# Performance work log

Hardware: AMD Instinct MI355X
Metric: run time of the kernel (lower is better)

## Reference

```python
import jax, jax.numpy as jnp
import numpy as np

D_MODEL = 1024
N_HEADS = 16
HEAD_DIM = D_MODEL // N_HEADS
SEQ_LEN = 2048
BATCH = 2
THETA = 10000.0


def _rope_tables(dim, seq_len, theta=THETA):
    freqs = 1.0 / theta ** (jnp.arange(0, dim, 2, dtype=jnp.float32) / dim)  # (dim/2,)
    t = jnp.arange(seq_len, dtype=jnp.float32)
    ang = jnp.outer(t, freqs)  # (S, dim/2)
    # interleave each freq twice to match the (-x_odd, x_even) rotation layout
    cos = jnp.repeat(jnp.cos(ang), 2, axis=-1)  # (S, dim)
    sin = jnp.repeat(jnp.sin(ang), 2, axis=-1)
    return cos, sin


def _apply_rope(x, cos, sin):
    # x: (B, S, H, D); cos/sin: (S, D)
    x_rot = jnp.stack([-x[..., 1::2], x[..., ::2]], axis=-1).reshape(x.shape)
    return x * cos[None, :, None, :] + x_rot * sin[None, :, None, :]


def setup_inputs() -> dict:
    key = jax.random.key(0)
    ks = jax.random.split(key, 9)
    s = 1.0 / np.sqrt(D_MODEL)
    return {
        "x": jax.random.normal(ks[0], (BATCH, SEQ_LEN, D_MODEL), dtype=jnp.float32),
        "wq": jax.random.normal(ks[1], (D_MODEL, D_MODEL), jnp.float32) * s,
        "bq": jnp.zeros((D_MODEL,), jnp.float32),
        "wk": jax.random.normal(ks[2], (D_MODEL, D_MODEL), jnp.float32) * s,
        "bk": jnp.zeros((D_MODEL,), jnp.float32),
        "wv": jax.random.normal(ks[3], (D_MODEL, D_MODEL), jnp.float32) * s,
        "bv": jnp.zeros((D_MODEL,), jnp.float32),
        "wo": jax.random.normal(ks[4], (D_MODEL, D_MODEL), jnp.float32) * s,
        "bo": jnp.zeros((D_MODEL,), jnp.float32),
    }


def reference(x, wq, bq, wk, bk, wv, bv, wo, bo):
    B, S, _ = x.shape
    cos, sin = _rope_tables(HEAD_DIM, S)
    # projections (torch Linear: x @ W^T + b)
    q = (x @ wq.T + bq).reshape(B, S, N_HEADS, HEAD_DIM)
    k = (x @ wk.T + bk).reshape(B, S, N_HEADS, HEAD_DIM)
    v = (x @ wv.T + bv).reshape(B, S, N_HEADS, HEAD_DIM)
    q = _apply_rope(q, cos, sin)
    k = _apply_rope(k, cos, sin)
    # attention: bhqd, bhkd -> bhqk
    scale = 1.0 / np.sqrt(HEAD_DIM)
    scores = jnp.einsum("bqhd,bkhd->bhqk", q, k) * scale
    attn = jax.nn.softmax(scores, axis=-1)
    out = jnp.einsum("bhqk,bkhd->bqhd", attn, v).reshape(B, S, D_MODEL)
    return out @ wo.T + bo
```

## Files before the change

kernel.cpp:

```cpp
#include <hip/hip_runtime.h>

typedef __attribute__((ext_vector_type(8))) __bf16 bf16x8;
typedef __attribute__((ext_vector_type(4))) __bf16 bf16x4;
typedef __attribute__((ext_vector_type(4))) float f32x4;
typedef __attribute__((ext_vector_type(16))) float f32x16;
typedef __attribute__((ext_vector_type(4))) int i32x4;
typedef __attribute__((ext_vector_type(4))) unsigned short ushort4v;

__device__ __forceinline__ unsigned short f2bf(float f) {
  unsigned u = __builtin_bit_cast(unsigned, f);
  u += 0x7fffu + ((u >> 16) & 1u);
  return (unsigned short)(u >> 16);
}

__device__ __forceinline__ unsigned cvt_pk_bf16(float lo, float hi) {
  unsigned r;
  asm("v_cvt_pk_bf16_f32 %0, %1, %2" : "=v"(r) : "v"(lo), "v"(hi));
  return r;
}

__device__ __forceinline__ void pl32swap(unsigned& a, unsigned& b) {
  asm("v_permlane32_swap_b32 %0, %1" : "+v"(a), "+v"(b));
}

__device__ __forceinline__ void gload16(const void* g, void* l) {
  __builtin_amdgcn_global_load_lds(
      (const __attribute__((address_space(1))) void*)g,
      (__attribute__((address_space(3))) void*)l, 16, 0, 0);
}

__global__ __launch_bounds__(256) void convert_k(
    const float* __restrict__ x, const float* __restrict__ wq,
    const float* __restrict__ wk, const float* __restrict__ wv,
    const float* __restrict__ wo,
    unsigned short* __restrict__ xb, unsigned short* __restrict__ wqkv,
    unsigned short* __restrict__ wob, float* cosT, float* sinT) {
  if (blockIdx.x >= 8192) {
    const int idx = (blockIdx.x - 8192) * 256 + threadIdx.x;
    const int s = idx >> 5, j = idx & 31;
    const float freq = powf(10000.f, -(float)(2 * j) * (1.f / 64.f));
    const float ang = (float)s * freq;
    cosT[idx] = cosf(ang);
    sinT[idx] = sinf(ang);
    return;
  }
  const size_t i = ((size_t)blockIdx.x * 256 + threadIdx.x) * 4;
  const float* src; unsigned short* dst; size_t off;
  if (i < 4194304)      { src = x;  dst = xb;              off = i; }
  else if (i < 5242880) { src = wq; dst = wqkv;            off = i - 4194304; }
  else if (i < 6291456) { src = wk; dst = wqkv + 1048576;  off = i - 5242880; }
  else if (i < 7340032) { src = wv; dst = wqkv + 2097152;  off = i - 6291456; }
  else                  { src = wo; dst = wob;             off = i - 7340032; }
  f32x4 v = *(const f32x4*)(src + off);
  ushort4v o;
  o[0] = f2bf(v[0]); o[1] = f2bf(v[1]); o[2] = f2bf(v[2]); o[3] = f2bf(v[3]);
  *(ushort4v*)(dst + off) = o;
}

template <int EPI>
__global__ __launch_bounds__(256) void gemm_bt_k(
    const unsigned short* __restrict__ A, const unsigned short* __restrict__ B,
    int M, int N, int K,
    unsigned short* __restrict__ Qr, unsigned short* __restrict__ Kr,
    unsigned short* __restrict__ Vt,
    const float* __restrict__ bq, const float* __restrict__ bk,
    const float* __restrict__ bvv,
    const float* __restrict__ cosT, const float* __restrict__ sinT,
    float* __restrict__ Cout, const float* __restrict__ bias) {
  __shared__ char smem[65536];
  const int t = threadIdx.x;
  const int wave = t >> 6, lane = t & 63;
  const int l15 = lane & 15, g = lane >> 4;
  const int cpx = (int)gridDim.x >> 3;
  const int wg = (blockIdx.x & 7) * cpx + (blockIdx.x >> 3);
  const int nt = N >> 7;
  const int mb = (wg / nt) << 7;
  const int nb = (wg % nt) << 7;
  const int wm = (wave >> 1) << 6;
  const int wn = (wave & 1) << 6;

  const f32x4 zv = {0.f, 0.f, 0.f, 0.f};
  f32x4 acc[4][4];
#pragma unroll
  for (int i = 0; i < 4; i++)
#pragma unroll
    for (int j = 0; j < 4; j++) acc[i][j] = zv;

#pragma unroll
  for (int i = 0; i < 4; i++) {
    const int lin = t * 16 + i * 4096;
    const int r = lin >> 7;
    const int cb = (lin & 127) ^ ((r & 7) << 4);
    gload16((const char*)A + ((size_t)(mb + r) * K) * 2 + cb,
            smem + i * 4096 + wave * 1024);
    gload16((const char*)B + ((size_t)(nb + r) * K) * 2 + cb,
            smem + 16384 + i * 4096 + wave * 1024);
  }
  __syncthreads();

  int cur = 0;
  for (int kt = 0; kt < K; kt += 64) {
    const char* sc = smem + cur * 32768;
    if (kt + 64 < K) {
      char* sn = smem + (cur ^ 1) * 32768;
#pragma unroll
      for (int i = 0; i < 4; i++) {
        const int lin = t * 16 + i * 4096;
        const int r = lin >> 7;
        const int cb = (lin & 127) ^ ((r & 7) << 4);
        gload16((const char*)A + ((size_t)(mb + r) * K + kt + 64) * 2 + cb,
                sn + i * 4096 + wave * 1024);
        gload16((const char*)B + ((size_t)(nb + r) * K + kt + 64) * 2 + cb,
                sn + 16384 + i * 4096 + wave * 1024);
      }
    }

    bf16x8 af[4][2], bfr[4][2];
    const int sw = (l15 & 7) << 4;
#pragma unroll
    for (int mf = 0; mf < 4; mf++) {
      const int r = wm + mf * 16 + l15;
      const int r2 = wn + mf * 16 + l15;
#pragma unroll
      for (int kf = 0; kf < 2; kf++) {
        af[mf][kf]  = *(const bf16x8*)(sc + r * 128 + ((kf * 64 + g * 16) ^ sw));
        bfr[mf][kf] = *(const bf16x8*)(sc + 16384 + r2 * 128 + ((kf * 64 + g * 16) ^ sw));
      }
    }
#pragma unroll
    for (int mf = 0; mf < 4; mf++)
#pragma unroll
      for (int nf = 0; nf < 4; nf++) {
        acc[mf][nf] = __builtin_amdgcn_mfma_f32_16x16x32_bf16(af[mf][0], bfr[nf][0], acc[mf][nf], 0, 0, 0);
        acc[mf][nf] = __builtin_amdgcn_mfma_f32_16x16x32_bf16(af[mf][1], bfr[nf][1], acc[mf][nf], 0, 0, 0);
      }
    __syncthreads();
    cur ^= 1;
  }

#pragma unroll
  for (int mf = 0; mf < 4; mf++) {
#pragma unroll
    for (int nf = 0; nf < 4; nf++) {
      const int row0 = mb + wm + mf * 16 + g * 4;
      const int col = nb + wn + nf * 16 + l15;
      if (EPI == 1) {
        const float bsv = bias[col];
#pragma unroll
        for (int r = 0; r < 4; r++)
          Cout[(size_t)(row0 + r) * N + col] = acc[mf][nf][r] + bsv;
      } else {
        const int region = col >> 10;
        const int cc = col & 1023;
        const int h = cc >> 6, d = cc & 63;
        const float bias_v = (region == 0 ? bq : (region == 1 ? bk : bvv))[cc];
        if (region < 2) {
          unsigned short* Ob = (region == 0 ? Qr : Kr);
          const float scl = (region == 0) ? 0.180336880111120425f : 1.0f;
#pragma unroll
          for (int r = 0; r < 4; r++) {
            const int row = row0 + r;
            const int s = row & 2047;
            const int b = row >> 11;
            const float v = acc[mf][nf][r] + bias_v;
            const float p = __shfl_xor(v, 1);
            const float c = cosT[s * 32 + (d >> 1)];
            const float sn = sinT[s * 32 + (d >> 1)];
            float o = (d & 1) ? (v * c + p * sn) : (v * c - p * sn);
            o *= scl;
            Ob[((size_t)(b * 16 + h) * 2048 + s) * 64 + d] = f2bf(o);
          }
        } else {
          ushort4v w;
#pragma unroll
          for (int r = 0; r < 4; r++) w[r] = f2bf(acc[mf][nf][r] + bias_v);
          const int s = row0 & 2047;
          const int b = row0 >> 11;
          *(ushort4v*)(Vt + ((size_t)(b * 16 + h) * 64 + d) * 2048 + s) = w;
        }
      }
    }
  }
}

__global__ __launch_bounds__(256, 4) void flash_k(
    const unsigned short* __restrict__ Qr, const unsigned short* __restrict__ Kr,
    const unsigned short* __restrict__ Vt, unsigned short* __restrict__ Op,
    float* __restrict__ Lp) {
  __shared__ char smem[32768];
  const int bid = blockIdx.x;
  const int bh = ((bid & 7) << 2) | ((bid >> 3) & 3);
  const int rest = bid >> 5;
  const int qt = rest & 15;
  const int ck = rest >> 4;
  const int kvb = ck << 10;
  const int t = threadIdx.x;
  const int wave = t >> 6, lane = t & 63;
  const int l31 = lane & 31, h32 = lane >> 5;
  const int q0 = qt * 128 + wave * 32;
  const unsigned short* Qb = Qr + ((size_t)bh * 2048 + q0) * 64;
  const char* Kb = (const char*)(Kr + (size_t)bh * 2048 * 64);
  const char* Vb = (const char*)(Vt + (size_t)bh * 64 * 2048);

  bf16x8 qB[4];
#pragma unroll
  for (int t4 = 0; t4 < 4; t4++)
    qB[t4] = *(const bf16x8*)(Qb + l31 * 64 + t4 * 16 + h32 * 8);

  const f32x16 z16 = {0,0,0,0,0,0,0,0,0,0,0,0,0,0,0,0};
  f32x16 ot0 = z16, ot1 = z16;
  float lsum = 0.f;
  const int swv = (l31 & 7) << 4;

#pragma unroll
  for (int i = 0; i < 2; i++) {
    const int lin = t * 16 + i * 4096;
    const int r = lin >> 7;
    const int cb = (lin & 127) ^ ((r & 7) << 4);
    gload16(Kb + (size_t)(kvb + r) * 128 + cb, smem + i * 4096 + wave * 1024);
    gload16(Vb + (size_t)r * 4096 + kvb * 2 + cb, smem + 8192 + i * 4096 + wave * 1024);
  }
  __syncthreads();

  for (int it = 0; it < 16; ++it) {
    const char* kb = smem + (it & 1) * 16384;
    const char* vbuf = kb + 8192;
    if (it < 15) {
      const int kvn = kvb + ((it + 1) << 6);
      char* kd = smem + ((it & 1) ^ 1) * 16384;
#pragma unroll
      for (int i = 0; i < 2; i++) {
        const int lin = t * 16 + i * 4096;
        const int r = lin >> 7;
        const int cb = (lin & 127) ^ ((r & 7) << 4);
        gload16(Kb + (size_t)(kvn + r) * 128 + cb, kd + i * 4096 + wave * 1024);
        gload16(Vb + (size_t)r * 4096 + kvn * 2 + cb, kd + 8192 + i * 4096 + wave * 1024);
      }
    }
    f32x16 st0 = z16, st1 = z16;
#pragma unroll
    for (int t4 = 0; t4 < 4; t4++) {
      const bf16x8 ka0 = *(const bf16x8*)(kb + l31 * 128 + ((t4 * 32 + h32 * 16) ^ swv));
      const bf16x8 ka1 = *(const bf16x8*)(kb + (32 + l31) * 128 + ((t4 * 32 + h32 * 16) ^ swv));
      st0 = __builtin_amdgcn_mfma_f32_32x32x16_bf16(ka0, qB[t4], st0, 0, 0, 0);
      st1 = __builtin_amdgcn_mfma_f32_32x32x16_bf16(ka1, qB[t4], st1, 0, 0, 0);
    }
    float ls0 = 0.f, ls1 = 0.f;
#pragma unroll
    for (int e = 0; e < 16; e++) {
      const float p0 = __builtin_amdgcn_exp2f(st0[e] - 16.0f);
      const float p1 = __builtin_amdgcn_exp2f(st1[e] - 16.0f);
      st0[e] = p0; st1[e] = p1;
      ls0 += p0; ls1 += p1;
    }
    lsum += ls0 + ls1;
#pragma unroll
    for (int tile = 0; tile < 2; tile++) {
      const f32x16& s = tile ? st1 : st0;
#pragma unroll
      for (int sg = 0; sg < 2; sg++) {
        unsigned b0 = cvt_pk_bf16(s[8 * sg + 0], s[8 * sg + 1]);
        unsigned b1 = cvt_pk_bf16(s[8 * sg + 2], s[8 * sg + 3]);
        unsigned b2 = cvt_pk_bf16(s[8 * sg + 4], s[8 * sg + 5]);
        unsigned b3 = cvt_pk_bf16(s[8 * sg + 6], s[8 * sg + 7]);
        pl32swap(b0, b2);
        pl32swap(b1, b3);
        const i32x4 bw = {(int)b0, (int)b1, (int)b2, (int)b3};
        const bf16x8 pb = __builtin_bit_cast(bf16x8, bw);
        const int kvbyte = tile * 64 + sg * 32 + h32 * 16;
        const bf16x8 va0 = *(const bf16x8*)(vbuf + l31 * 128 + (kvbyte ^ swv));
        const bf16x8 va1 = *(const bf16x8*)(vbuf + (32 + l31) * 128 + (kvbyte ^ swv));
        ot0 = __builtin_amdgcn_mfma_f32_32x32x16_bf16(va0, pb, ot0, 0, 0, 0);
        ot1 = __builtin_amdgcn_mfma_f32_32x32x16_bf16(va1, pb, ot1, 0, 0, 0);
      }
    }
    __syncthreads();
  }
  lsum += __shfl_xor(lsum, 32);
  const size_t obase = (((size_t)(ck * 32 + bh)) * 2048 + q0 + l31) * 64;
#pragma unroll
  for (int dt = 0; dt < 2; dt++) {
#pragma unroll
    for (int grp = 0; grp < 4; grp++) {
      bf16x4 w;
#pragma unroll
      for (int e = 0; e < 4; e++)
        w[e] = (__bf16)(dt ? ot1[grp * 4 + e] : ot0[grp * 4 + e]);
      *(bf16x4*)(Op + obase + dt * 32 + grp * 8 + 4 * h32) = w;
    }
  }
  if (lane < 32)
    Lp[((size_t)(ck * 32 + bh)) * 2048 + q0 + l31] = lsum;
}

__global__ __launch_bounds__(256) void reduce_k(
    const unsigned short* __restrict__ Op, const float* __restrict__ Lp,
    unsigned short* __restrict__ Oa) {
  const size_t o = ((size_t)blockIdx.x * 256 + threadIdx.x) * 8;
  const int d0 = (int)(o & 63);
  const int h  = (int)((o >> 6) & 15);
  const int s  = (int)((o >> 10) & 2047);
  const int b  = (int)(o >> 21);
  const size_t pi = (((size_t)(b * 16 + h)) * 2048 + s) * 64 + d0;
  const size_t li = ((size_t)(b * 16 + h)) * 2048 + s;
  const bf16x8 a = *(const bf16x8*)(Op + pi);
  const bf16x8 c = *(const bf16x8*)(Op + pi + 4194304);
  const float inv = 1.f / (Lp[li] + Lp[li + 65536]);
  bf16x8 w;
#pragma unroll
  for (int e = 0; e < 8; e++)
    w[e] = (__bf16)(((float)a[e] + (float)c[e]) * inv);
  *(bf16x8*)(Oa + o) = w;
}

extern "C" void kernel_launch(void* const* d_in, const int* in_sizes, int n_in,
                              void* d_out, int out_size, void* d_ws, size_t ws_size,
                              hipStream_t stream) {
  const float* x  = (const float*)d_in[0];
  const float* wq = (const float*)d_in[1];
  const float* bq = (const float*)d_in[2];
  const float* wk = (const float*)d_in[3];
  const float* bk = (const float*)d_in[4];
  const float* wv = (const float*)d_in[5];
  const float* bv = (const float*)d_in[6];
  const float* wo = (const float*)d_in[7];
  const float* bo = (const float*)d_in[8];
  float* out = (float*)d_out;
  char* ws = (char*)d_ws;

  unsigned short* xb    = (unsigned short*)(ws);
  unsigned short* wqkv  = (unsigned short*)(ws + 8388608);
  float* cosT           = (float*)(ws + 14680064);
  float* sinT           = (float*)(ws + 14942208);
  unsigned short* Opart = (unsigned short*)(ws);
  unsigned short* Qr    = (unsigned short*)(ws + 16777216);
  unsigned short* Oa    = (unsigned short*)(ws + 16777216);
  unsigned short* Kr    = (unsigned short*)(ws + 25165824);
  unsigned short* Vt    = (unsigned short*)(ws + 33554432);
  unsigned short* wob   = (unsigned short*)(ws + 41943040);
  float* Lpart          = (float*)(ws + 44040192);

  convert_k<<<dim3(8448), dim3(256), 0, stream>>>(x, wq, wk, wv, wo, xb, wqkv, wob, cosT, sinT);
  gemm_bt_k<0><<<dim3(32 * 24), dim3(256), 0, stream>>>(
      xb, wqkv, 4096, 3072, 1024, Qr, Kr, Vt, bq, bk, bv, cosT, sinT,
      (float*)nullptr, (const float*)nullptr);
  flash_k<<<dim3(1024), dim3(256), 0, stream>>>(Qr, Kr, Vt, Opart, Lpart);
  reduce_k<<<dim3(2048), dim3(256), 0, stream>>>(Opart, Lpart, Oa);
  gemm_bt_k<1><<<dim3(32 * 8), dim3(256), 0, stream>>>(
      Oa, wob, 4096, 1024, 1024,
      (unsigned short*)nullptr, (unsigned short*)nullptr, (unsigned short*)nullptr,
      (const float*)nullptr, (const float*)nullptr, (const float*)nullptr,
      cosT, sinT, out, bo);
}
```

Measured before the change: 122.1 us.

## Switch GEMM to 512-thread blocks with single-buffered LDS

The projection GEMMs now run 8 waves per 128x128 tile, each computing 64x32, instead of 4 waves computing 64x64. The LDS double buffer and prefetch of the next K tile are dropped. Each iteration now loads, syncs, computes and syncs with a 32KB single buffer. This halves per-wave accumulator registers and raises waves per block, which may help occupancy. In exchange, global-load latency is no longer overlapped with MFMA work inside a block.

```diff
diff --git a/kernel.cpp b/kernel.cpp
--- a/kernel.cpp
+++ b/kernel.cpp
@@ -58,7 +58,7 @@
 }
 
 template <int EPI>
-__global__ __launch_bounds__(256) void gemm_bt_k(
+__global__ __launch_bounds__(512) void gemm_bt_k(
     const unsigned short* __restrict__ A, const unsigned short* __restrict__ B,
     int M, int N, int K,
     unsigned short* __restrict__ Qr, unsigned short* __restrict__ Kr,
@@ -67,7 +67,7 @@
     const float* __restrict__ bvv,
     const float* __restrict__ cosT, const float* __restrict__ sinT,
     float* __restrict__ Cout, const float* __restrict__ bias) {
-  __shared__ char smem[65536];
+  __shared__ char smem[32768];
   const int t = threadIdx.x;
   const int wave = t >> 6, lane = t & 63;
   const int l15 = lane & 15, g = lane >> 4;
@@ -76,72 +76,59 @@
   const int nt = N >> 7;
   const int mb = (wg / nt) << 7;
   const int nb = (wg % nt) << 7;
-  const int wm = (wave >> 1) << 6;
-  const int wn = (wave & 1) << 6;
+  const int wm = (wave >> 2) << 6;
+  const int wn = (wave & 3) << 5;
 
   const f32x4 zv = {0.f, 0.f, 0.f, 0.f};
-  f32x4 acc[4][4];
+  f32x4 acc[4][2];
 #pragma unroll
   for (int i = 0; i < 4; i++)
 #pragma unroll
-    for (int j = 0; j < 4; j++) acc[i][j] = zv;
-
-#pragma unroll
-  for (int i = 0; i < 4; i++) {
-    const int lin = t * 16 + i * 4096;
-    const int r = lin >> 7;
-    const int cb = (lin & 127) ^ ((r & 7) << 4);
-    gload16((const char*)A + ((size_t)(mb + r) * K) * 2 + cb,
-            smem + i * 4096 + wave * 1024);
-    gload16((const char*)B + ((size_t)(nb + r) * K) * 2 + cb,
-            smem + 16384 + i * 4096 + wave * 1024);
-  }
-  __syncthreads();
-
-  int cur = 0;
+    for (int j = 0; j < 2; j++) acc[i][j] = zv;
+
   for (int kt = 0; kt < K; kt += 64) {
-    const char* sc = smem + cur * 32768;
-    if (kt + 64 < K) {
-      char* sn = smem + (cur ^ 1) * 32768;
-#pragma unroll
-      for (int i = 0; i < 4; i++) {
-        const int lin = t * 16 + i * 4096;
-        const int r = lin >> 7;
-        const int cb = (lin & 127) ^ ((r & 7) << 4);
-        gload16((const char*)A + ((size_t)(mb + r) * K + kt + 64) * 2 + cb,
-                sn + i * 4096 + wave * 1024);
-        gload16((const char*)B + ((size_t)(nb + r) * K + kt + 64) * 2 + cb,
-                sn + 16384 + i * 4096 + wave * 1024);
-      }
-    }
-
-    bf16x8 af[4][2], bfr[4][2];
+#pragma unroll
+    for (int i = 0; i < 2; i++) {
+      const int lin = t * 16 + i * 8192;
+      const int r = lin >> 7;
+      const int cb = (lin & 127) ^ ((r & 7) << 4);
+      gload16((const char*)A + ((size_t)(mb + r) * K + kt) * 2 + cb,
+              smem + i * 8192 + wave * 1024);
+      gload16((const char*)B + ((size_t)(nb + r) * K + kt) * 2 + cb,
+              smem + 16384 + i * 8192 + wave * 1024);
+    }
+    __syncthreads();
+
+    bf16x8 af[4][2], bfr[2][2];
     const int sw = (l15 & 7) << 4;
 #pragma unroll
     for (int mf = 0; mf < 4; mf++) {
       const int r = wm + mf * 16 + l15;
-      const int r2 = wn + mf * 16 + l15;
-#pragma unroll
-      for (int kf = 0; kf < 2; kf++) {
-        af[mf][kf]  = *(const bf16x8*)(sc + r * 128 + ((kf * 64 + g * 16) ^ sw));
-        bfr[mf][kf] = *(const bf16x8*)(sc + 16384 + r2 * 128 + ((kf * 64 + g * 16) ^ sw));
-      }
+#pragma unroll
+      for (int kf = 0; kf < 2; kf++)
+        af[mf][kf] = *(const bf16x8*)(smem + r * 128 + ((kf * 64 + g * 16) ^ sw));
+    }
+#pragma unroll
+    for (int nf = 0; nf < 2; nf++) {
+      const int r2 = wn + nf * 16 + l15;
+#pragma unroll
+      for (int kf = 0; kf < 2; kf++)
+        bfr[nf][kf] = *(const bf16x8*)(smem + 16384 + r2 * 128 + ((kf * 64 + g * 16) ^ sw));
     }
 #pragma unroll
     for (int mf = 0; mf < 4; mf++)
 #pragma unroll
-      for (int nf = 0; nf < 4; nf++) {
+      for (int nf = 0; nf < 2; nf++) {
         acc[mf][nf] = __builtin_amdgcn_mfma_f32_16x16x32_bf16(af[mf][0], bfr[nf][0], acc[mf][nf], 0, 0, 0);
         acc[mf][nf] = __builtin_amdgcn_mfma_f32_16x16x32_bf16(af[mf][1], bfr[nf][1], acc[mf][nf], 0, 0, 0);
       }
     __syncthreads();
-    cur ^= 1;
   }
 
 #pragma unroll
   for (int mf = 0; mf < 4; mf++) {
 #pragma unroll
-    for (int nf = 0; nf < 4; nf++) {
+    for (int nf = 0; nf < 2; nf++) {
       const int row0 = mb + wm + mf * 16 + g * 4;
       const int col = nb + wn + nf * 16 + l15;
       if (EPI == 1) {
@@ -341,12 +328,12 @@
   float* Lpart          = (float*)(ws + 44040192);
 
   convert_k<<<dim3(8448), dim3(256), 0, stream>>>(x, wq, wk, wv, wo, xb, wqkv, wob, cosT, sinT);
-  gemm_bt_k<0><<<dim3(32 * 24), dim3(256), 0, stream>>>(
+  gemm_bt_k<0><<<dim3(32 * 24), dim3(512), 0, stream>>>(
       xb, wqkv, 4096, 3072, 1024, Qr, Kr, Vt, bq, bk, bv, cosT, sinT,
       (float*)nullptr, (const float*)nullptr);
   flash_k<<<dim3(1024), dim3(256), 0, stream>>>(Qr, Kr, Vt, Opart, Lpart);
   reduce_k<<<dim3(2048), dim3(256), 0, stream>>>(Opart, Lpart, Oa);
-  gemm_bt_k<1><<<dim3(32 * 8), dim3(256), 0, stream>>>(
+  gemm_bt_k<1><<<dim3(32 * 8), dim3(512), 0, stream>>>(
       Oa, wob, 4096, 1024, 1024,
       (unsigned short*)nullptr, (unsigned short*)nullptr, (unsigned short*)nullptr,
       (const float*)nullptr, (const float*)nullptr, (const float*)nullptr,
```

New measurement: 119.2 us. -2.4%, faster.
